# Optimization experiments

Hardware: AMD Instinct MI355X
Metric: run time of the kernel (lower is better)

## Reference

```python
import jax, jax.numpy as jnp
import numpy as np

N = 50000   # nodes
E = 800000  # edges (before self-loops)
DIN = 128
H, C = 4, 32
HC = H * C  # 128
DE = 3      # edge feature dim
G = 64      # graphs in batch
HID = 32
DOUT = 1
LN_EPS = 1e-5


def setup_inputs() -> dict:
    key = jax.random.key(0)
    ks = iter(jax.random.split(key, 64))
    def nrm(shape, s=0.1):
        return jax.random.normal(next(ks), shape, dtype=jnp.float32) * s
    inp = {}
    inp["x"] = jax.random.normal(next(ks), (N, DIN), dtype=jnp.float32)
    inp["edge_index"] = jax.random.randint(next(ks), (2, E), 0, N, dtype=jnp.int32)
    inp["batch"] = jnp.sort(jax.random.randint(next(ks), (N,), 0, G, dtype=jnp.int32))
    inp["edge_attr"] = jax.random.normal(next(ks), (E, DE), dtype=jnp.float32)
    # GATv2 layers: layer0 in=DIN(128); layers 1,2 in=HC(128)
    for l, din in enumerate([DIN, HC, HC]):
        inp[f"Wl{l}"] = nrm((HC, din)); inp[f"bl{l}"] = jnp.zeros((HC,), jnp.float32)
        inp[f"Wr{l}"] = nrm((HC, din)); inp[f"br{l}"] = jnp.zeros((HC,), jnp.float32)
        inp[f"We{l}"] = nrm((HC, DE))
        inp[f"att{l}"] = nrm((H, C))
        inp[f"bo{l}"] = jnp.zeros((HC,), jnp.float32)
    for l in range(2):
        inp[f"ln{l}_g"] = jnp.ones((HC,), jnp.float32)
        inp[f"ln{l}_b"] = jnp.zeros((HC,), jnp.float32)
    # post-processing MLP: 128->32->32->32->1
    inp["pw1"] = nrm((HID, HC)); inp["pb1"] = jnp.zeros((HID,), jnp.float32)
    inp["pw2"] = nrm((HID, HID)); inp["pb2"] = jnp.zeros((HID,), jnp.float32)
    inp["pw3"] = nrm((HID, HID)); inp["pb3"] = jnp.zeros((HID,), jnp.float32)
    inp["pw4"] = nrm((DOUT, HID)); inp["pb4"] = jnp.zeros((DOUT,), jnp.float32)
    return inp


def _gat_layer(x, src, dst, eattr, Wl, bl, Wr, br, We, att, bo):
    # GATv2Conv (concat heads). x_l from lin_l -> source, x_r from lin_r -> target.
    xl = (x @ Wl.T + bl).reshape(-1, H, C)
    xr = (x @ Wr.T + br).reshape(-1, H, C)
    e = (eattr @ We.T).reshape(-1, H, C)
    m = jax.nn.leaky_relu(xl[src] + xr[dst] + e, negative_slope=0.2)  # [E',H,C]
    s = jnp.einsum('ehc,hc->eh', m, att)                              # [E',H]
    smax = jax.ops.segment_max(s, dst, num_segments=N)
    ex = jnp.exp(s - smax[dst])
    den = jax.ops.segment_sum(ex, dst, num_segments=N)
    alpha = ex / (den[dst] + 1e-16)
    out = jax.ops.segment_sum(alpha[:, :, None] * xl[src], dst, num_segments=N)
    return out.reshape(-1, HC) + bo


def _ln(x, g, b):
    mu = jnp.mean(x, axis=-1, keepdims=True)
    var = jnp.mean((x - mu) ** 2, axis=-1, keepdims=True)
    return (x - mu) * jax.lax.rsqrt(var + LN_EPS) * g + b


def _forward(x, edge_attr, edge_index, batch, p):
    src0, dst0 = edge_index[0], edge_index[1]
    # PyG add_self_loops with fill_value='mean': per-dst-node mean of edge_attr
    cnt = jax.ops.segment_sum(jnp.ones((E,), jnp.float32), dst0, num_segments=N)
    loop_attr = jax.ops.segment_sum(edge_attr, dst0, num_segments=N) / jnp.maximum(cnt, 1.0)[:, None]
    ar = jnp.arange(N, dtype=src0.dtype)
    src = jnp.concatenate([src0, ar]); dst = jnp.concatenate([dst0, ar])
    ea = jnp.concatenate([edge_attr, loop_attr], axis=0)
    embedding = x
    for l in range(3):
        x = _gat_layer(x, src, dst, ea, p[f"Wl{l}"], p[f"bl{l}"], p[f"Wr{l}"],
                       p[f"br{l}"], p[f"We{l}"], p[f"att{l}"], p[f"bo{l}"])
        embedding = x
        x = jax.nn.relu(x)  # dropout inactive (eval)
        if l != 2:
            x = _ln(x, p[f"ln{l}_g"], p[f"ln{l}_b"])
    pooled = jax.ops.segment_max(x, batch, num_segments=G)
    pooled = jnp.where(jnp.isfinite(pooled), pooled, 0.0)
    h = jax.nn.relu(pooled @ p["pw1"].T + p["pb1"])
    h = jax.nn.relu(h @ p["pw2"].T + p["pb2"])
    h = jax.nn.relu(h @ p["pw3"].T + p["pb3"])
    out = h @ p["pw4"].T + p["pb4"]
    return embedding, out


def reference(x, edge_index, batch, edge_attr,
              Wl0, bl0, Wr0, br0, We0, att0, bo0,
              Wl1, bl1, Wr1, br1, We1, att1, bo1,
              Wl2, bl2, Wr2, br2, We2, att2, bo2,
              ln0_g, ln0_b, ln1_g, ln1_b,
              pw1, pb1, pw2, pb2, pw3, pb3, pw4, pb4):
    p = dict(Wl0=Wl0, bl0=bl0, Wr0=Wr0, br0=br0, We0=We0, att0=att0, bo0=bo0,
             Wl1=Wl1, bl1=bl1, Wr1=Wr1, br1=br1, We1=We1, att1=att1, bo1=bo1,
             Wl2=Wl2, bl2=bl2, Wr2=Wr2, br2=br2, We2=We2, att2=att2, bo2=bo2,
             ln0_g=ln0_g, ln0_b=ln0_b, ln1_g=ln1_g, ln1_b=ln1_b,
             pw1=pw1, pb1=pb1, pw2=pw2, pb2=pb2, pw3=pw3, pb3=pb3, pw4=pw4, pb4=pb4)
    return _forward(x, edge_attr, edge_index, batch, p)
```

## Files before the change

### kernel.cpp

```cpp
#include <hip/hip_runtime.h>
#include <math.h>


#define LN_EPS 1e-5f
#define LOG2E 1.44269504088896340736f

typedef short bf16x8 __attribute__((ext_vector_type(8)));
typedef float f32x4 __attribute__((ext_vector_type(4)));

static __device__ __forceinline__ unsigned short f2bf(float f) {
  unsigned int u = __float_as_uint(f);
  u += 0x7fffu + ((u >> 16) & 1u);
  return (unsigned short)(u >> 16);
}

static __device__ __forceinline__ float dpp_sum8(float v) {
  int x;
  x = __builtin_amdgcn_update_dpp(0, __float_as_int(v), 0x0B1, 0xf, 0xf, true);
  v += __int_as_float(x);
  x = __builtin_amdgcn_update_dpp(0, __float_as_int(v), 0x04E, 0xf, 0xf, true);
  v += __int_as_float(x);
  x = __builtin_amdgcn_update_dpp(0, __float_as_int(v), 0x141, 0xf, 0xf, true);
  v += __int_as_float(x);
  return v;
}


__global__ void k_degree(const int* __restrict__ ei, int* __restrict__ cnt, int E) {
  int e = (blockIdx.x * blockDim.x + threadIdx.x) * 4;
  if (e + 3 < E) {
    int4 d = *(const int4*)&ei[E + e];
    atomicAdd(&cnt[d.x], 1);
    atomicAdd(&cnt[d.y], 1);
    atomicAdd(&cnt[d.z], 1);
    atomicAdd(&cnt[d.w], 1);
  } else {
    int lim = min(e + 4, E);
    for (; e < lim; ++e) atomicAdd(&cnt[ei[E + e]], 1);
  }
}

__global__ void k_scan1(const int* __restrict__ cnt, int* __restrict__ bsum, int N) {
  __shared__ int sh[256];
  int t = threadIdx.x;
  int n = blockIdx.x * 256 + t;
  sh[t] = (n < N) ? (cnt[n] + 1) : 0;
  __syncthreads();
  for (int s = 128; s > 0; s >>= 1) {
    if (t < s) sh[t] += sh[t + s];
    __syncthreads();
  }
  if (t == 0) bsum[blockIdx.x] = sh[0];
}

__global__ void k_scan2(int* __restrict__ bsum, int* __restrict__ offs, int nb, int total, int N) {
  __shared__ int sh[256];
  int t = threadIdx.x;
  int v = (t < nb) ? bsum[t] : 0;
  sh[t] = v;
  __syncthreads();
  for (int d = 1; d < 256; d <<= 1) {
    int add = (t >= d) ? sh[t - d] : 0;
    __syncthreads();
    sh[t] += add;
    __syncthreads();
  }
  if (t < nb) bsum[t] = sh[t] - v;
  if (t == 0) offs[N] = total;
}

__global__ void k_scan3(const int* __restrict__ cnt, const int* __restrict__ bsum,
                        int* __restrict__ offs, int N) {
  __shared__ int sh[256];
  int t = threadIdx.x;
  int n = blockIdx.x * 256 + t;
  int v = (n < N) ? (cnt[n] + 1) : 0;
  sh[t] = v;
  __syncthreads();
  for (int d = 1; d < 256; d <<= 1) {
    int add = (t >= d) ? sh[t - d] : 0;
    __syncthreads();
    sh[t] += add;
    __syncthreads();
  }
  if (n < N) offs[n] = bsum[blockIdx.x] + sh[t] - v;
}

__global__ void k_initcur(const int* __restrict__ offs, int* __restrict__ gcur, int nbuk) {
  int t = threadIdx.x;
  if (t < nbuk) gcur[t] = offs[t * 256];
}

#define CHUNK 4096
__global__ __launch_bounds__(256) void k_binA(const int* __restrict__ ei, const float* __restrict__ ea,
                                              int* __restrict__ gcur, float4* __restrict__ staged,
                                              int E, int nbuk) {
  __shared__ int hist[256];
  __shared__ int basebuf[256];
  int t = threadIdx.x;
  int e0 = blockIdx.x * CHUNK;

  hist[t] = 0;
  __syncthreads();
#pragma unroll
  for (int i = 0; i < CHUNK / 256; ++i) {
    int e = e0 + i * 256 + t;
    if (e < E) atomicAdd(&hist[ei[E + e] >> 8], 1);
  }
  __syncthreads();
  int h = hist[t];
  if (t < nbuk && h > 0) basebuf[t] = atomicAdd(&gcur[t], h);
  hist[t] = 0;
  __syncthreads();
#pragma unroll
  for (int i = 0; i < CHUNK / 256; ++i) {
    int e = e0 + i * 256 + t;
    if (e < E) {
      int s = ei[e];
      int d = ei[E + e];
      int b = d >> 8;
      int r = atomicAdd(&hist[b], 1);
      float4 rec;
      rec.x = ea[e * 3 + 0];
      rec.y = ea[e * 3 + 1];
      rec.z = ea[e * 3 + 2];
      rec.w = __int_as_float(s | (d << 16));
      staged[basebuf[b] + r] = rec;
    }
  }
}

__global__ __launch_bounds__(256) void k_binB(const float4* __restrict__ staged,
                                              const int* __restrict__ offs,
                                              float4* __restrict__ e4, int N) {
  __shared__ int cur[256];
  int t = threadIdx.x;
  int n0 = blockIdx.x * 256;
  int n1 = min(n0 + 256, N);
  if (n0 + t < n1) cur[t] = offs[n0 + t];
  int start = offs[n0];
  int cntReal = (offs[n1] - start) - (n1 - n0);
  __syncthreads();
  for (int p = start + t; p < start + cntReal; p += 256) {
    float4 rec = staged[p];
    unsigned int u = (unsigned int)__float_as_int(rec.w);
    int s = (int)(u & 0xffffu);
    int d = (int)(u >> 16);
    int pos = atomicAdd(&cur[d - n0], 1);
    float4 out;
    out.x = rec.x;
    out.y = rec.y;
    out.z = rec.z;
    out.w = __int_as_float(s * 256);
    e4[pos] = out;
  }
}

__global__ void k_selfloop(const int* __restrict__ offs, float4* __restrict__ e4, int N) {
  int idx = blockIdx.x * blockDim.x + threadIdx.x;
  int n = idx >> 2;
  if (n >= N) return;
  int sub = idx & 3;
  int beg = offs[n], last = offs[n + 1] - 1;
  float s0 = 0.f, s1 = 0.f, s2 = 0.f;
  for (int p = beg + sub; p < last; p += 4) {
    float4 v = e4[p];
    s0 += v.x;
    s1 += v.y;
    s2 += v.z;
  }
  s0 += __shfl_xor(s0, 1);
  s1 += __shfl_xor(s1, 1);
  s2 += __shfl_xor(s2, 1);
  s0 += __shfl_xor(s0, 2);
  s1 += __shfl_xor(s1, 2);
  s2 += __shfl_xor(s2, 2);
  if (sub == 0) {
    float invc = 1.0f / fmaxf((float)(last - beg), 1.0f);
    float4 r;
    r.x = s0 * invc;
    r.y = s1 * invc;
    r.z = s2 * invc;
    r.w = __int_as_float(n * 256);
    e4[last] = r;
  }
}


__global__ void k_convx(const float* __restrict__ x, unsigned short* __restrict__ xb, int n) {
  int i = (blockIdx.x * blockDim.x + threadIdx.x) * 4;
  if (i >= n) return;
  float4 v = *(const float4*)&x[i];
  ushort4 o;
  o.x = f2bf(v.x); o.y = f2bf(v.y); o.z = f2bf(v.z); o.w = f2bf(v.w);
  *(ushort4*)&xb[i] = o;
}

__global__ void k_convW(const float* __restrict__ w0, const float* __restrict__ w1,
                        const float* __restrict__ w2, const float* __restrict__ w3,
                        const float* __restrict__ w4, const float* __restrict__ w5,
                        unsigned short* __restrict__ dst) {
  const float* srcs[6] = {w0, w1, w2, w3, w4, w5};
  const float* s = srcs[blockIdx.y];
  int i = blockIdx.x * 256 + threadIdx.x;
  dst[(size_t)blockIdx.y * 16384 + i] = f2bf(s[i]);
}

__global__ __launch_bounds__(256) void k_gemm_mfma(const unsigned short* __restrict__ xb,
                                                   const unsigned short* __restrict__ Wb,
                                                   const float* __restrict__ bl, const float* __restrict__ br,
                                                   unsigned short* __restrict__ xlb,
                                                   unsigned short* __restrict__ xrb, int N) {
  int wave = threadIdx.x >> 6;
  int lane = threadIdx.x & 63;
  int which = blockIdx.y;
  const unsigned short* W = Wb + (size_t)which * 16384;
  const float* bias = which ? br : bl;
  unsigned short* out = which ? xrb : xlb;

  int row0 = (blockIdx.x * 4 + wave) * 16;
  if (row0 >= N) return;
  int m = lane & 15;
  int q = lane >> 4;

  int arow = row0 + m;
  if (arow >= N) arow = N - 1;
  const unsigned short* xrow = xb + (size_t)arow * 128 + q * 8;

  bf16x8 afrag[4];
#pragma unroll
  for (int kt = 0; kt < 4; ++kt) afrag[kt] = *(const bf16x8*)(xrow + kt * 32);

  f32x4 acc[8];
#pragma unroll
  for (int jt = 0; jt < 8; ++jt) acc[jt] = (f32x4){0.f, 0.f, 0.f, 0.f};

  const unsigned short* wbase = W + (size_t)m * 128 + q * 8;
#pragma unroll
  for (int kt = 0; kt < 4; ++kt) {
    bf16x8 a = afrag[kt];
#pragma unroll
    for (int jt = 0; jt < 8; ++jt) {
      bf16x8 b = *(const bf16x8*)(wbase + (size_t)jt * 16 * 128 + kt * 32);
      acc[jt] = __builtin_amdgcn_mfma_f32_16x16x32_bf16(a, b, acc[jt], 0, 0, 0);
    }
  }

#pragma unroll
  for (int jt = 0; jt < 8; ++jt) {
    float bs = bias[jt * 16 + m];
#pragma unroll
    for (int r = 0; r < 4; ++r) {
      int rr = row0 + q * 4 + r;
      if (rr < N) out[(size_t)rr * 128 + jt * 16 + m] = f2bf(acc[jt][r] + bs);
    }
  }
}

__global__ __launch_bounds__(256) void k_agg(const unsigned short* __restrict__ xlb,
                                             const unsigned short* __restrict__ xrb,
                                             const float4* __restrict__ e4,
                                             const int* __restrict__ offs,
                                             const float* __restrict__ We, const float* __restrict__ att,
                                             const float* __restrict__ bo,
                                             const float* __restrict__ lng, const float* __restrict__ lnb,
                                             unsigned short* __restrict__ xnext_bf,
                                             float* __restrict__ emb, int last, int N) {
  int w = (blockIdx.x * blockDim.x + threadIdx.x) >> 6;
  if (w >= N) return;
  int lane = threadIdx.x & 63;
  int half = lane >> 5;
  int sl = lane & 31;
  int c = sl * 4;
  unsigned int c2 = (unsigned int)(c * 2);
  int beg = offs[w], end = offs[w + 1];
  int cnt = end - beg;

  f32x4 xr4, wea, web, wec, at4;
  {
    uint2 vr = *(const uint2*)&xrb[(size_t)w * 128 + c];
    xr4[0] = __uint_as_float(vr.x << 16);
    xr4[1] = __uint_as_float(vr.x & 0xffff0000u);
    xr4[2] = __uint_as_float(vr.y << 16);
    xr4[3] = __uint_as_float(vr.y & 0xffff0000u);
#pragma unroll
    for (int j = 0; j < 4; ++j) {
      wea[j] = We[(c + j) * 3 + 0];
      web[j] = We[(c + j) * 3 + 1];
      wec[j] = We[(c + j) * 3 + 2];
      at4[j] = att[c + j] * LOG2E;
    }
  }

  const char* xlB = (const char*)xlb;
  const char* e4B = (const char*)e4;
  unsigned int lastoff = (unsigned int)(end - 1) << 4;
  unsigned int eoff = (unsigned int)(beg + half) << 4;
  if (eoff > lastoff) eoff = lastoff;

  float l = 0.f;
  f32x4 acc = {0.f, 0.f, 0.f, 0.f};

  int T = (cnt + 1) >> 1;
  float4 eC = *(const float4*)(e4B + eoff);

#pragma unroll 2
  for (int it = 0; it < T - 1; ++it) {
    unsigned int noff = eoff + 32u;
    if (noff > lastoff) noff = lastoff;
    float4 eN = *(const float4*)(e4B + noff);
    eoff = noff;

    unsigned int go = (unsigned int)__float_as_int(eC.w) + c2;
    uint2 v = *(const uint2*)(xlB + go);
    f32x4 xl4;
    xl4[0] = __uint_as_float(v.x << 16);
    xl4[1] = __uint_as_float(v.x & 0xffff0000u);
    xl4[2] = __uint_as_float(v.y << 16);
    xl4[3] = __uint_as_float(v.y & 0xffff0000u);

    f32x4 t = xr4 + wea * eC.x + web * eC.y + wec * eC.z + xl4;
    t[0] = fmaxf(t[0], 0.2f * t[0]);
    t[1] = fmaxf(t[1], 0.2f * t[1]);
    t[2] = fmaxf(t[2], 0.2f * t[2]);
    t[3] = fmaxf(t[3], 0.2f * t[3]);
    float s = t[0] * at4[0] + t[1] * at4[1] + t[2] * at4[2] + t[3] * at4[3];
    float wgt = __builtin_amdgcn_exp2f(dpp_sum8(s));
    l += wgt;
    acc += xl4 * wgt;
    eC = eN;
  }
  {
    int idx = 2 * (T - 1) + half;
    unsigned int go = (unsigned int)__float_as_int(eC.w) + c2;
    uint2 v = *(const uint2*)(xlB + go);
    f32x4 xl4;
    xl4[0] = __uint_as_float(v.x << 16);
    xl4[1] = __uint_as_float(v.x & 0xffff0000u);
    xl4[2] = __uint_as_float(v.y << 16);
    xl4[3] = __uint_as_float(v.y & 0xffff0000u);
    f32x4 t = xr4 + wea * eC.x + web * eC.y + wec * eC.z + xl4;
    t[0] = fmaxf(t[0], 0.2f * t[0]);
    t[1] = fmaxf(t[1], 0.2f * t[1]);
    t[2] = fmaxf(t[2], 0.2f * t[2]);
    t[3] = fmaxf(t[3], 0.2f * t[3]);
    float s = t[0] * at4[0] + t[1] * at4[1] + t[2] * at4[2] + t[3] * at4[3];
    float wgt = __builtin_amdgcn_exp2f(dpp_sum8(s));
    if (idx >= cnt) wgt = 0.f;
    l += wgt;
    acc += xl4 * wgt;
  }

  l += __shfl_xor(l, 32);
  acc[0] += __shfl_xor(acc[0], 32);
  acc[1] += __shfl_xor(acc[1], 32);
  acc[2] += __shfl_xor(acc[2], 32);
  acc[3] += __shfl_xor(acc[3], 32);

  float inv = 1.0f / l;
  f32x4 o;
  const float4 bo4 = *(const float4*)&bo[c];
  o[0] = acc[0] * inv + bo4.x;
  o[1] = acc[1] * inv + bo4.y;
  o[2] = acc[2] * inv + bo4.z;
  o[3] = acc[3] * inv + bo4.w;

  if (last) {
    if (half == 0) {
      float4 st = {o[0], o[1], o[2], o[3]};
      *(float4*)&emb[(size_t)w * 128 + c] = st;
    }
  } else {
    f32x4 r;
    r[0] = fmaxf(o[0], 0.f);
    r[1] = fmaxf(o[1], 0.f);
    r[2] = fmaxf(o[2], 0.f);
    r[3] = fmaxf(o[3], 0.f);
    float s = r[0] + r[1] + r[2] + r[3];
    s += __shfl_xor(s, 1);
    s += __shfl_xor(s, 2);
    s += __shfl_xor(s, 4);
    s += __shfl_xor(s, 8);
    s += __shfl_xor(s, 16);
    float mu = s * 0.0078125f;
    f32x4 d;
    d[0] = r[0] - mu;
    d[1] = r[1] - mu;
    d[2] = r[2] - mu;
    d[3] = r[3] - mu;
    float v2 = d[0] * d[0] + d[1] * d[1] + d[2] * d[2] + d[3] * d[3];
    v2 += __shfl_xor(v2, 1);
    v2 += __shfl_xor(v2, 2);
    v2 += __shfl_xor(v2, 4);
    v2 += __shfl_xor(v2, 8);
    v2 += __shfl_xor(v2, 16);
    float var = v2 * 0.0078125f;
    float rstd = rsqrtf(var + LN_EPS);
    if (half == 0) {
      const float4 g4 = *(const float4*)&lng[c];
      const float4 b4 = *(const float4*)&lnb[c];
      float o0 = d[0] * rstd * g4.x + b4.x;
      float o1 = d[1] * rstd * g4.y + b4.y;
      float o2 = d[2] * rstd * g4.z + b4.z;
      float o3 = d[3] * rstd * g4.w + b4.w;
      uint2 pack;
      pack.x = (unsigned int)f2bf(o0) | ((unsigned int)f2bf(o1) << 16);
      pack.y = (unsigned int)f2bf(o2) | ((unsigned int)f2bf(o3) << 16);
      *(uint2*)&xnext_bf[(size_t)w * 128 + c] = pack;
    }
  }
}

__global__ void k_pool(const float* __restrict__ emb, const int* __restrict__ batch,
                       float* __restrict__ pooled, int N) {
  int c = threadIdx.x & 127;
  int half = threadIdx.x >> 7;
  int base = blockIdx.x * 64 + half;
  int limit = min(blockIdx.x * 64 + 64, N);
  float cur = 0.f;
  int curg = -1;
  for (int n = base; n < limit; n += 2) {
    int g = batch[n];
    if (g != curg) {
      if (curg >= 0) atomicMax((unsigned int*)&pooled[curg * 128 + c], __float_as_uint(cur));
      curg = g;
      cur = 0.f;
    }
    cur = fmaxf(cur, emb[(size_t)n * 128 + c]);
  }
  if (curg >= 0) atomicMax((unsigned int*)&pooled[curg * 128 + c], __float_as_uint(cur));
}

__global__ void k_mlp(const float* __restrict__ pooled,
                      const float* __restrict__ pw1, const float* __restrict__ pb1,
                      const float* __restrict__ pw2, const float* __restrict__ pb2,
                      const float* __restrict__ pw3, const float* __restrict__ pb3,
                      const float* __restrict__ pw4, const float* __restrict__ pb4,
                      float* __restrict__ out) {
  int g = blockIdx.x;
  int t = threadIdx.x;
  __shared__ float buf1[32], buf2[32];
  if (t < 32) {
    float acc = pb1[t];
    for (int k = 0; k < 128; ++k) acc += pw1[t * 128 + k] * pooled[g * 128 + k];
    buf1[t] = fmaxf(acc, 0.f);
  }
  __syncthreads();
  if (t < 32) {
    float acc = pb2[t];
    for (int k = 0; k < 32; ++k) acc += pw2[t * 32 + k] * buf1[k];
    buf2[t] = fmaxf(acc, 0.f);
  }
  __syncthreads();
  if (t < 32) {
    float acc = pb3[t];
    for (int k = 0; k < 32; ++k) acc += pw3[t * 32 + k] * buf2[k];
    buf1[t] = fmaxf(acc, 0.f);
  }
  __syncthreads();
  if (t == 0) {
    float acc = pb4[0];
    for (int k = 0; k < 32; ++k) acc += pw4[k] * buf1[k];
    out[g] = acc;
  }
}


extern "C" void kernel_launch(void* const* d_in, const int* in_sizes, int n_in,
                              void* d_out, int out_size, void* d_ws, size_t ws_size,
                              hipStream_t stream) {
  const float* x_in = (const float*)d_in[0];
  const int* ei = (const int*)d_in[1];
  const int* batch = (const int*)d_in[2];
  const float* ea = (const float*)d_in[3];

  const int N = in_sizes[0] / 128;
  const int E = in_sizes[1] / 2;
  const int EP = E + N;
  const int G = out_size - N * 128;
  const int NBUK = (N + 255) / 256;

  const float *Wl[3], *bl[3], *Wr[3], *br[3], *We[3], *att[3], *bo[3];
  for (int l = 0; l < 3; ++l) {
    Wl[l] = (const float*)d_in[4 + 7 * l];
    bl[l] = (const float*)d_in[5 + 7 * l];
    Wr[l] = (const float*)d_in[6 + 7 * l];
    br[l] = (const float*)d_in[7 + 7 * l];
    We[l] = (const float*)d_in[8 + 7 * l];
    att[l] = (const float*)d_in[9 + 7 * l];
    bo[l] = (const float*)d_in[10 + 7 * l];
  }
  const float* lng[2] = {(const float*)d_in[25], (const float*)d_in[27]};
  const float* lnb[2] = {(const float*)d_in[26], (const float*)d_in[28]};
  const float* pw1 = (const float*)d_in[29];
  const float* pb1 = (const float*)d_in[30];
  const float* pw2 = (const float*)d_in[31];
  const float* pb2 = (const float*)d_in[32];
  const float* pw3 = (const float*)d_in[33];
  const float* pb3 = (const float*)d_in[34];
  const float* pw4 = (const float*)d_in[35];
  const float* pb4 = (const float*)d_in[36];

  char* base = (char*)d_ws;
  size_t cur = 0;
  auto carve = [&](size_t bytes) -> char* {
    char* p = base + cur;
    cur += (bytes + 255) & ~(size_t)255;
    return p;
  };
  unsigned short* xlb = (unsigned short*)carve((size_t)N * 128 * 2);
  unsigned short* xrb = (unsigned short*)carve((size_t)N * 128 * 2);
  unsigned short* xb = (unsigned short*)carve((size_t)N * 128 * 2);
  unsigned short* Wb = (unsigned short*)carve((size_t)6 * 16384 * 2);
  float4* e4 = (float4*)carve((size_t)EP * 16);
  float4* staged = (float4*)carve((size_t)EP * 16);
  int* offs = (int*)carve((size_t)(N + 1) * 4);
  int* cnt = (int*)carve((size_t)N * 4);
  int* gcur = (int*)carve((size_t)(NBUK + 1) * 4);
  int* bsum = (int*)carve(1024);
  float* pooled = (float*)carve((size_t)G * 128 * 4);

  float* emb_out = (float*)d_out;
  float* mlp_out = (float*)d_out + (size_t)N * 128;

  const int NB = (N + 255) / 256;

  hipMemsetAsync(cnt, 0, (size_t)N * 4, stream);
  hipMemsetAsync(pooled, 0, (size_t)G * 128 * 4, stream);

  k_degree<<<(E / 4 + 255) / 256, 256, 0, stream>>>(ei, cnt, E);
  k_scan1<<<NB, 256, 0, stream>>>(cnt, bsum, N);
  k_scan2<<<1, 256, 0, stream>>>(bsum, offs, NB, EP, N);
  k_scan3<<<NB, 256, 0, stream>>>(cnt, bsum, offs, N);
  k_initcur<<<1, 256, 0, stream>>>(offs, gcur, NBUK);
  k_binA<<<(E + CHUNK - 1) / CHUNK, 256, 0, stream>>>(ei, ea, gcur, staged, E, NBUK);
  k_binB<<<NBUK, 256, 0, stream>>>(staged, offs, e4, N);
  k_selfloop<<<(N * 4 + 255) / 256, 256, 0, stream>>>(offs, e4, N);

  k_convx<<<(N * 128 / 4 + 255) / 256, 256, 0, stream>>>(x_in, xb, N * 128);
  {
    dim3 g(64, 6);
    k_convW<<<g, 256, 0, stream>>>(Wl[0], Wr[0], Wl[1], Wr[1], Wl[2], Wr[2], Wb);
  }

  for (int l = 0; l < 3; ++l) {
    dim3 ggrid((N + 63) / 64, 2);
    k_gemm_mfma<<<ggrid, 256, 0, stream>>>(xb, Wb + (size_t)l * 32768, bl[l], br[l], xlb, xrb, N);
    int last = (l == 2) ? 1 : 0;
    const float* g = last ? bo[l] : lng[l];
    const float* b = last ? bo[l] : lnb[l];
    k_agg<<<(N * 64 + 255) / 256, 256, 0, stream>>>(xlb, xrb, e4, offs,
                                                    We[l], att[l], bo[l], g, b,
                                                    xb, emb_out, last, N);
  }

  k_pool<<<(N + 63) / 64, 256, 0, stream>>>(emb_out, batch, pooled, N);
  k_mlp<<<G, 64, 0, stream>>>(pooled, pw1, pb1, pw2, pb2, pw3, pb3, pw4, pb4, mlp_out);
}
```

Before: 530.2 us.

## Restructure CSR build into fixed-capacity buckets, swap GEMM operands, prepack score weights

Drops the separate degree count and three scan kernels. Edges are now binned into fixed-capacity per-bucket staging slots, so k_binB can build per-node offsets locally and compute the self-loop edge features in the same kernel. The MFMA GEMM swaps its A and B operands so each lane holds consecutive output columns, which allows packed 8-byte bf16 stores and vector bias loads. A small kernel prepacks We and att into a per-lane table so the aggregation kernel loads them with four float4 reads. This assumes no bucket holds more than 8192 edges (BCAP), and the self-loop mean is now a serial loop per thread.

```diff
diff --git a/kernel.cpp b/kernel.cpp
--- a/kernel.cpp
+++ b/kernel.cpp
@@ -4,6 +4,8 @@
 
 #define LN_EPS 1e-5f
 #define LOG2E 1.44269504088896340736f
+#define CHUNK 4096
+#define BCAP 8192
 
 typedef short bf16x8 __attribute__((ext_vector_type(8)));
 typedef float f32x4 __attribute__((ext_vector_type(4)));
@@ -26,74 +28,8 @@
 }
 
 
-__global__ void k_degree(const int* __restrict__ ei, int* __restrict__ cnt, int E) {
-  int e = (blockIdx.x * blockDim.x + threadIdx.x) * 4;
-  if (e + 3 < E) {
-    int4 d = *(const int4*)&ei[E + e];
-    atomicAdd(&cnt[d.x], 1);
-    atomicAdd(&cnt[d.y], 1);
-    atomicAdd(&cnt[d.z], 1);
-    atomicAdd(&cnt[d.w], 1);
-  } else {
-    int lim = min(e + 4, E);
-    for (; e < lim; ++e) atomicAdd(&cnt[ei[E + e]], 1);
-  }
-}
-
-__global__ void k_scan1(const int* __restrict__ cnt, int* __restrict__ bsum, int N) {
-  __shared__ int sh[256];
-  int t = threadIdx.x;
-  int n = blockIdx.x * 256 + t;
-  sh[t] = (n < N) ? (cnt[n] + 1) : 0;
-  __syncthreads();
-  for (int s = 128; s > 0; s >>= 1) {
-    if (t < s) sh[t] += sh[t + s];
-    __syncthreads();
-  }
-  if (t == 0) bsum[blockIdx.x] = sh[0];
-}
-
-__global__ void k_scan2(int* __restrict__ bsum, int* __restrict__ offs, int nb, int total, int N) {
-  __shared__ int sh[256];
-  int t = threadIdx.x;
-  int v = (t < nb) ? bsum[t] : 0;
-  sh[t] = v;
-  __syncthreads();
-  for (int d = 1; d < 256; d <<= 1) {
-    int add = (t >= d) ? sh[t - d] : 0;
-    __syncthreads();
-    sh[t] += add;
-    __syncthreads();
-  }
-  if (t < nb) bsum[t] = sh[t] - v;
-  if (t == 0) offs[N] = total;
-}
-
-__global__ void k_scan3(const int* __restrict__ cnt, const int* __restrict__ bsum,
-                        int* __restrict__ offs, int N) {
-  __shared__ int sh[256];
-  int t = threadIdx.x;
-  int n = blockIdx.x * 256 + t;
-  int v = (n < N) ? (cnt[n] + 1) : 0;
-  sh[t] = v;
-  __syncthreads();
-  for (int d = 1; d < 256; d <<= 1) {
-    int add = (t >= d) ? sh[t - d] : 0;
-    __syncthreads();
-    sh[t] += add;
-    __syncthreads();
-  }
-  if (n < N) offs[n] = bsum[blockIdx.x] + sh[t] - v;
-}
-
-__global__ void k_initcur(const int* __restrict__ offs, int* __restrict__ gcur, int nbuk) {
-  int t = threadIdx.x;
-  if (t < nbuk) gcur[t] = offs[t * 256];
-}
-
-#define CHUNK 4096
 __global__ __launch_bounds__(256) void k_binA(const int* __restrict__ ei, const float* __restrict__ ea,
-                                              int* __restrict__ gcur, float4* __restrict__ staged,
+                                              int* __restrict__ gcnt, float4* __restrict__ staged,
                                               int E, int nbuk) {
   __shared__ int hist[256];
   __shared__ int basebuf[256];
@@ -109,7 +45,7 @@
   }
   __syncthreads();
   int h = hist[t];
-  if (t < nbuk && h > 0) basebuf[t] = atomicAdd(&gcur[t], h);
+  if (t < nbuk && h > 0) basebuf[t] = t * BCAP + atomicAdd(&gcnt[t], h);
   hist[t] = 0;
   __syncthreads();
 #pragma unroll
@@ -130,58 +66,83 @@
   }
 }
 
+__global__ void k_bscan(const int* __restrict__ gcnt, int* __restrict__ bukStart,
+                        int* __restrict__ offs, int N, int nbuk, int EP) {
+  __shared__ int sh[256];
+  int t = threadIdx.x;
+  int nodes = (t < nbuk) ? min(256, N - t * 256) : 0;
+  int v = (t < nbuk) ? gcnt[t] + nodes : 0;
+  sh[t] = v;
+  __syncthreads();
+  for (int d = 1; d < 256; d <<= 1) {
+    int add = (t >= d) ? sh[t - d] : 0;
+    __syncthreads();
+    sh[t] += add;
+    __syncthreads();
+  }
+  if (t < nbuk) bukStart[t] = sh[t] - v;
+  if (t == 0) offs[N] = EP;
+}
+
 __global__ __launch_bounds__(256) void k_binB(const float4* __restrict__ staged,
-                                              const int* __restrict__ offs,
-                                              float4* __restrict__ e4, int N) {
-  __shared__ int cur[256];
+                                              const int* __restrict__ gcnt,
+                                              const int* __restrict__ bukStart,
+                                              float4* __restrict__ e4,
+                                              int* __restrict__ offs, int N) {
+  __shared__ int hist[256], cur[256], begS[256], sh[256];
   int t = threadIdx.x;
-  int n0 = blockIdx.x * 256;
-  int n1 = min(n0 + 256, N);
-  if (n0 + t < n1) cur[t] = offs[n0 + t];
-  int start = offs[n0];
-  int cntReal = (offs[n1] - start) - (n1 - n0);
-  __syncthreads();
-  for (int p = start + t; p < start + cntReal; p += 256) {
-    float4 rec = staged[p];
+  int b = blockIdx.x;
+  int n0 = b * 256;
+  int nn = min(256, N - n0);
+  int m = gcnt[b];
+  size_t sbase = (size_t)b * BCAP;
+
+  hist[t] = 0;
+  __syncthreads();
+  for (int p = t; p < m; p += 256) {
+    unsigned int u = (unsigned int)__float_as_int(staged[sbase + p].w);
+    atomicAdd(&hist[(int)(u >> 16) - n0], 1);
+  }
+  __syncthreads();
+  int v = (t < nn) ? hist[t] + 1 : 0;
+  sh[t] = v;
+  __syncthreads();
+  for (int d = 1; d < 256; d <<= 1) {
+    int add = (t >= d) ? sh[t - d] : 0;
+    __syncthreads();
+    sh[t] += add;
+    __syncthreads();
+  }
+  if (t < nn) {
+    int base = bukStart[b] + sh[t] - v;
+    cur[t] = base;
+    begS[t] = base;
+    offs[n0 + t] = base;
+  }
+  __syncthreads();
+  for (int p = t; p < m; p += 256) {
+    float4 rec = staged[sbase + p];
     unsigned int u = (unsigned int)__float_as_int(rec.w);
-    int s = (int)(u & 0xffffu);
-    int d = (int)(u >> 16);
-    int pos = atomicAdd(&cur[d - n0], 1);
-    float4 out;
-    out.x = rec.x;
-    out.y = rec.y;
-    out.z = rec.z;
-    out.w = __int_as_float(s * 256);
-    e4[pos] = out;
-  }
-}
-
-__global__ void k_selfloop(const int* __restrict__ offs, float4* __restrict__ e4, int N) {
-  int idx = blockIdx.x * blockDim.x + threadIdx.x;
-  int n = idx >> 2;
-  if (n >= N) return;
-  int sub = idx & 3;
-  int beg = offs[n], last = offs[n + 1] - 1;
-  float s0 = 0.f, s1 = 0.f, s2 = 0.f;
-  for (int p = beg + sub; p < last; p += 4) {
-    float4 v = e4[p];
-    s0 += v.x;
-    s1 += v.y;
-    s2 += v.z;
-  }
-  s0 += __shfl_xor(s0, 1);
-  s1 += __shfl_xor(s1, 1);
-  s2 += __shfl_xor(s2, 1);
-  s0 += __shfl_xor(s0, 2);
-  s1 += __shfl_xor(s1, 2);
-  s2 += __shfl_xor(s2, 2);
-  if (sub == 0) {
+    int pos = atomicAdd(&cur[(int)(u >> 16) - n0], 1);
+    rec.w = __int_as_float((int)(u & 0xffffu) * 256);
+    e4[pos] = rec;
+  }
+  __syncthreads();
+  if (t < nn) {
+    int beg = begS[t], last = cur[t];
+    float s0 = 0.f, s1 = 0.f, s2 = 0.f;
+    for (int p = beg; p < last; ++p) {
+      float4 r = e4[p];
+      s0 += r.x;
+      s1 += r.y;
+      s2 += r.z;
+    }
     float invc = 1.0f / fmaxf((float)(last - beg), 1.0f);
     float4 r;
     r.x = s0 * invc;
     r.y = s1 * invc;
     r.z = s2 * invc;
-    r.w = __int_as_float(n * 256);
+    r.w = __int_as_float((n0 + t) * 256);
     e4[last] = r;
   }
 }
@@ -204,6 +165,24 @@
   const float* s = srcs[blockIdx.y];
   int i = blockIdx.x * 256 + threadIdx.x;
   dst[(size_t)blockIdx.y * 16384 + i] = f2bf(s[i]);
+}
+
+__global__ void k_pack(const float* __restrict__ We0, const float* __restrict__ att0,
+                       const float* __restrict__ We1, const float* __restrict__ att1,
+                       const float* __restrict__ We2, const float* __restrict__ att2,
+                       float* __restrict__ tab) {
+  int l = blockIdx.x;
+  int t = threadIdx.x;
+  const float* We = (l == 0) ? We0 : ((l == 1) ? We1 : We2);
+  const float* att = (l == 0) ? att0 : ((l == 1) ? att1 : att2);
+  float* o = tab + (size_t)l * 512 + t * 16;
+#pragma unroll
+  for (int j = 0; j < 4; ++j) {
+    o[j] = We[(t * 4 + j) * 3 + 0];
+    o[4 + j] = We[(t * 4 + j) * 3 + 1];
+    o[8 + j] = We[(t * 4 + j) * 3 + 2];
+    o[12 + j] = att[t * 4 + j] * LOG2E;
+  }
 }
 
 __global__ __launch_bounds__(256) void k_gemm_mfma(const unsigned short* __restrict__ xb,
@@ -223,13 +202,13 @@
   int m = lane & 15;
   int q = lane >> 4;
 
-  int arow = row0 + m;
-  if (arow >= N) arow = N - 1;
-  const unsigned short* xrow = xb + (size_t)arow * 128 + q * 8;
-
-  bf16x8 afrag[4];
-#pragma unroll
-  for (int kt = 0; kt < 4; ++kt) afrag[kt] = *(const bf16x8*)(xrow + kt * 32);
+  int brow = row0 + m;
+  if (brow >= N) brow = N - 1;
+  const unsigned short* xrow = xb + (size_t)brow * 128 + q * 8;
+
+  bf16x8 bfrag[4];
+#pragma unroll
+  for (int kt = 0; kt < 4; ++kt) bfrag[kt] = *(const bf16x8*)(xrow + kt * 32);
 
   f32x4 acc[8];
 #pragma unroll
@@ -238,21 +217,23 @@
   const unsigned short* wbase = W + (size_t)m * 128 + q * 8;
 #pragma unroll
   for (int kt = 0; kt < 4; ++kt) {
-    bf16x8 a = afrag[kt];
 #pragma unroll
     for (int jt = 0; jt < 8; ++jt) {
-      bf16x8 b = *(const bf16x8*)(wbase + (size_t)jt * 16 * 128 + kt * 32);
-      acc[jt] = __builtin_amdgcn_mfma_f32_16x16x32_bf16(a, b, acc[jt], 0, 0, 0);
-    }
-  }
-
-#pragma unroll
-  for (int jt = 0; jt < 8; ++jt) {
-    float bs = bias[jt * 16 + m];
-#pragma unroll
-    for (int r = 0; r < 4; ++r) {
-      int rr = row0 + q * 4 + r;
-      if (rr < N) out[(size_t)rr * 128 + jt * 16 + m] = f2bf(acc[jt][r] + bs);
+      bf16x8 a = *(const bf16x8*)(wbase + (size_t)jt * 16 * 128 + kt * 32);
+      acc[jt] = __builtin_amdgcn_mfma_f32_16x16x32_bf16(a, bfrag[kt], acc[jt], 0, 0, 0);
+    }
+  }
+
+  int node = row0 + m;
+  if (node < N) {
+    unsigned short* orow = out + (size_t)node * 128 + q * 4;
+#pragma unroll
+    for (int jt = 0; jt < 8; ++jt) {
+      float4 bs = *(const float4*)&bias[jt * 16 + q * 4];
+      uint2 pack;
+      pack.x = (unsigned int)f2bf(acc[jt][0] + bs.x) | ((unsigned int)f2bf(acc[jt][1] + bs.y) << 16);
+      pack.y = (unsigned int)f2bf(acc[jt][2] + bs.z) | ((unsigned int)f2bf(acc[jt][3] + bs.w) << 16);
+      *(uint2*)(orow + jt * 16) = pack;
     }
   }
 }
@@ -261,7 +242,7 @@
                                              const unsigned short* __restrict__ xrb,
                                              const float4* __restrict__ e4,
                                              const int* __restrict__ offs,
-                                             const float* __restrict__ We, const float* __restrict__ att,
+                                             const float* __restrict__ scoreTab,
                                              const float* __restrict__ bo,
                                              const float* __restrict__ lng, const float* __restrict__ lnb,
                                              unsigned short* __restrict__ xnext_bf,
@@ -278,18 +259,17 @@
 
   f32x4 xr4, wea, web, wec, at4;
   {
+    const float4* tp = (const float4*)(scoreTab + (size_t)sl * 16);
+    float4 pa = tp[0], pb = tp[1], pc = tp[2], pt = tp[3];
+    wea[0] = pa.x; wea[1] = pa.y; wea[2] = pa.z; wea[3] = pa.w;
+    web[0] = pb.x; web[1] = pb.y; web[2] = pb.z; web[3] = pb.w;
+    wec[0] = pc.x; wec[1] = pc.y; wec[2] = pc.z; wec[3] = pc.w;
+    at4[0] = pt.x; at4[1] = pt.y; at4[2] = pt.z; at4[3] = pt.w;
     uint2 vr = *(const uint2*)&xrb[(size_t)w * 128 + c];
     xr4[0] = __uint_as_float(vr.x << 16);
     xr4[1] = __uint_as_float(vr.x & 0xffff0000u);
     xr4[2] = __uint_as_float(vr.y << 16);
     xr4[3] = __uint_as_float(vr.y & 0xffff0000u);
-#pragma unroll
-    for (int j = 0; j < 4; ++j) {
-      wea[j] = We[(c + j) * 3 + 0];
-      web[j] = We[(c + j) * 3 + 1];
-      wec[j] = We[(c + j) * 3 + 2];
-      at4[j] = att[c + j] * LOG2E;
-    }
   }
 
   const char* xlB = (const char*)xlb;
@@ -513,35 +493,29 @@
   unsigned short* xb = (unsigned short*)carve((size_t)N * 128 * 2);
   unsigned short* Wb = (unsigned short*)carve((size_t)6 * 16384 * 2);
   float4* e4 = (float4*)carve((size_t)EP * 16);
-  float4* staged = (float4*)carve((size_t)EP * 16);
+  float4* staged = (float4*)carve((size_t)NBUK * BCAP * 16);
   int* offs = (int*)carve((size_t)(N + 1) * 4);
-  int* cnt = (int*)carve((size_t)N * 4);
-  int* gcur = (int*)carve((size_t)(NBUK + 1) * 4);
-  int* bsum = (int*)carve(1024);
+  int* gcnt = (int*)carve((size_t)NBUK * 4);
+  int* bukStart = (int*)carve((size_t)(NBUK + 1) * 4);
+  float* scoreTab = (float*)carve((size_t)3 * 512 * 4);
   float* pooled = (float*)carve((size_t)G * 128 * 4);
 
   float* emb_out = (float*)d_out;
   float* mlp_out = (float*)d_out + (size_t)N * 128;
 
-  const int NB = (N + 255) / 256;
-
-  hipMemsetAsync(cnt, 0, (size_t)N * 4, stream);
+  hipMemsetAsync(gcnt, 0, (size_t)NBUK * 4, stream);
   hipMemsetAsync(pooled, 0, (size_t)G * 128 * 4, stream);
 
-  k_degree<<<(E / 4 + 255) / 256, 256, 0, stream>>>(ei, cnt, E);
-  k_scan1<<<NB, 256, 0, stream>>>(cnt, bsum, N);
-  k_scan2<<<1, 256, 0, stream>>>(bsum, offs, NB, EP, N);
-  k_scan3<<<NB, 256, 0, stream>>>(cnt, bsum, offs, N);
-  k_initcur<<<1, 256, 0, stream>>>(offs, gcur, NBUK);
-  k_binA<<<(E + CHUNK - 1) / CHUNK, 256, 0, stream>>>(ei, ea, gcur, staged, E, NBUK);
-  k_binB<<<NBUK, 256, 0, stream>>>(staged, offs, e4, N);
-  k_selfloop<<<(N * 4 + 255) / 256, 256, 0, stream>>>(offs, e4, N);
+  k_binA<<<(E + CHUNK - 1) / CHUNK, 256, 0, stream>>>(ei, ea, gcnt, staged, E, NBUK);
+  k_bscan<<<1, 256, 0, stream>>>(gcnt, bukStart, offs, N, NBUK, EP);
+  k_binB<<<NBUK, 256, 0, stream>>>(staged, gcnt, bukStart, e4, offs, N);
 
   k_convx<<<(N * 128 / 4 + 255) / 256, 256, 0, stream>>>(x_in, xb, N * 128);
   {
     dim3 g(64, 6);
     k_convW<<<g, 256, 0, stream>>>(Wl[0], Wr[0], Wl[1], Wr[1], Wl[2], Wr[2], Wb);
   }
+  k_pack<<<3, 32, 0, stream>>>(We[0], att[0], We[1], att[1], We[2], att[2], scoreTab);
 
   for (int l = 0; l < 3; ++l) {
     dim3 ggrid((N + 63) / 64, 2);
@@ -550,7 +524,8 @@
     const float* g = last ? bo[l] : lng[l];
     const float* b = last ? bo[l] : lnb[l];
     k_agg<<<(N * 64 + 255) / 256, 256, 0, stream>>>(xlb, xrb, e4, offs,
-                                                    We[l], att[l], bo[l], g, b,
+                                                    scoreTab + (size_t)l * 512,
+                                                    bo[l], g, b,
                                                     xb, emb_out, last, N);
   }
 
```

Result: faster. 501.4 us (-5.4%).
